# Kernel tuning notes

Measured on AMD Instinct MI355X. Metric: run time of the kernel, lower is better.

The kernel has to match this reference:

```python
import jax, jax.numpy as jnp
import numpy as np


def setup_inputs() -> dict:
    key = jax.random.key(0)
    ks = jax.random.split(key, 7)
    B, V, D, H = 4, 1024, 3, 128
    vertices = jax.random.normal(ks[0], (B, V, D), dtype=jnp.float32)
    # Linear params (x @ W + b convention, W = torch_weight.T)
    W1 = jax.random.normal(ks[1], (2 * D, H), dtype=jnp.float32) * 0.05
    b1 = jnp.zeros((H,), dtype=jnp.float32)
    W2 = jax.random.normal(ks[2], (H, H // 2), dtype=jnp.float32) * 0.05
    b2 = jnp.zeros((H // 2,), dtype=jnp.float32)
    W3 = jax.random.normal(ks[3], (H // 2, 1), dtype=jnp.float32) * 0.05
    b3 = jnp.zeros((1,), dtype=jnp.float32)
    return {"vertices": vertices, "W1": W1, "b1": b1, "W2": W2, "b2": b2, "W3": W3, "b3": b3}


def reference(vertices, W1, b1, W2, b2, W3, b3):
    B, V, D = vertices.shape
    # All unordered pairs (i, j) with i < j -- same order as the nested loop.
    idx_i, idx_j = jnp.triu_indices(V, k=1)  # each [E], E = V*(V-1)/2
    # Pairwise edge features [B, E, 2D] via gather (no Python loop).
    edge_features = jnp.concatenate(
        [vertices[:, idx_i, :], vertices[:, idx_j, :]], axis=-1
    )
    # 3-layer MLP (dropout is identity in eval mode).
    x = jax.nn.relu(edge_features @ W1 + b1)   # [B, E, H]
    x = jax.nn.relu(x @ W2 + b2)               # [B, E, H//2]
    x = x @ W3 + b3                            # [B, E, 1]
    edge_probs = jax.nn.sigmoid(x[..., 0])     # [B, E]
    edge_indices = jnp.stack([idx_i, idx_j], axis=1)  # [E, 2]
    return edge_probs, edge_indices
```

## Files before the change

kernel.cpp:

```cpp
#include <hip/hip_runtime.h>
#include <hip/hip_bf16.h>
#include <math.h>

#define BB 4
#define VV 1024
#define HH 128
#define H2 64
#define EE 523776
#define BE (BB * EE)
#define TPB (EE / 16)
#define NTILES (BE / 16)
#define NTHR 256
#define NBLK 1024

typedef __attribute__((ext_vector_type(8))) short bf16x8;
typedef __attribute__((ext_vector_type(4))) float f32x4;

__device__ __forceinline__ short f2bf(float f) {
    __hip_bfloat16 h = __float2bfloat16(f);
    return *reinterpret_cast<short*>(&h);
}

__global__ __launch_bounds__(NTHR, 3) void edge_mlp_mfma2(
    const float* __restrict__ vertices,
    const float* __restrict__ W1,
    const float* __restrict__ b1,
    const float* __restrict__ W2,
    const float* __restrict__ b2,
    const float* __restrict__ W3,
    const float* __restrict__ b3,
    float* __restrict__ out)
{
    const int lane = threadIdx.x & 63;
    const int col  = lane & 15;
    const int u    = lane >> 4;
    const int wid  = threadIdx.x >> 6;

    const f32x4 zero4 = {0.f, 0.f, 0.f, 0.f};

    bf16x8 A1[4][2];
#pragma unroll
    for (int p = 0; p < 4; ++p)
#pragma unroll
        for (int q = 0; q < 2; ++q) {
            const int h = 32 * p + 8 * (col >> 2) + 4 * q + (col & 3);
#pragma unroll
            for (int r = 0; r < 8; ++r) {
                const int k = 8 * u + r;
                float w = 0.0f;
                if (k < 6)       w = W1[k * HH + h];
                else if (k == 6) w = b1[h];
                A1[p][q][r] = f2bf(w);
            }
        }

    bf16x8 A2[4][4];
#pragma unroll
    for (int mt = 0; mt < 4; ++mt)
#pragma unroll
        for (int p = 0; p < 4; ++p) {
            const int n2 = 16 * mt + col;
#pragma unroll
            for (int r = 0; r < 8; ++r) {
                const int h = 32 * p + 8 * u + r;
                A2[mt][p][r] = f2bf(W2[h * H2 + n2]);
            }
        }

    f32x4 cinit[4];
    float w3c[16];
#pragma unroll
    for (int mt = 0; mt < 4; ++mt)
#pragma unroll
        for (int q = 0; q < 4; ++q) {
            const int n2 = 16 * mt + 4 * u + q;
            cinit[mt][q]    = b2[n2];
            w3c[mt * 4 + q] = W3[n2];
        }
    const float b3v = b3[0];

    const int gw = blockIdx.x * 4 + wid;

    for (int tt = gw; tt < NTILES; tt += NBLK * 4) {
        const int b  = tt / TPB;
        const int e0 = (tt - b * TPB) * 16;
        const int e  = e0 + col;

        const int rr = EE - 1 - e;
        const float sq = sqrtf((float)(8 * rr + 1));
        int m = (int)(0.5f * (sq - 1.0f));
        if ((m + 1) * (m + 2) / 2 <= rr) ++m;
        if (m * (m + 1) / 2 > rr) --m;
        const int pp = rr - m * (m + 1) / 2;
        const int iv = VV - 2 - m;
        const int jv = VV - 1 - pp;

        bf16x8 bf = {0, 0, 0, 0, 0, 0, 0, 0};
        if (u == 0) {
            const float* pvi = vertices + (b * VV + iv) * 3;
            const float* pvj = vertices + (b * VV + jv) * 3;
            bf[0] = f2bf(pvi[0]); bf[1] = f2bf(pvi[1]); bf[2] = f2bf(pvi[2]);
            bf[3] = f2bf(pvj[0]); bf[4] = f2bf(pvj[1]); bf[5] = f2bf(pvj[2]);
            bf[6] = f2bf(1.0f);
        }

        f32x4 d2_0 = cinit[0], d2_1 = cinit[1], d2_2 = cinit[2], d2_3 = cinit[3];

#pragma unroll
        for (int p = 0; p < 4; ++p) {
            f32x4 dA = __builtin_amdgcn_mfma_f32_16x16x32_bf16(A1[p][0], bf, zero4, 0, 0, 0);
            f32x4 dB = __builtin_amdgcn_mfma_f32_16x16x32_bf16(A1[p][1], bf, zero4, 0, 0, 0);
            bf16x8 Bh;
            Bh[0] = f2bf(fmaxf(dA[0], 0.f)); Bh[1] = f2bf(fmaxf(dA[1], 0.f));
            Bh[2] = f2bf(fmaxf(dA[2], 0.f)); Bh[3] = f2bf(fmaxf(dA[3], 0.f));
            Bh[4] = f2bf(fmaxf(dB[0], 0.f)); Bh[5] = f2bf(fmaxf(dB[1], 0.f));
            Bh[6] = f2bf(fmaxf(dB[2], 0.f)); Bh[7] = f2bf(fmaxf(dB[3], 0.f));
            d2_0 = __builtin_amdgcn_mfma_f32_16x16x32_bf16(A2[0][p], Bh, d2_0, 0, 0, 0);
            d2_1 = __builtin_amdgcn_mfma_f32_16x16x32_bf16(A2[1][p], Bh, d2_1, 0, 0, 0);
            d2_2 = __builtin_amdgcn_mfma_f32_16x16x32_bf16(A2[2][p], Bh, d2_2, 0, 0, 0);
            d2_3 = __builtin_amdgcn_mfma_f32_16x16x32_bf16(A2[3][p], Bh, d2_3, 0, 0, 0);
        }

        float acc = 0.f;
#pragma unroll
        for (int q = 0; q < 4; ++q) acc = fmaf(fmaxf(d2_0[q], 0.f), w3c[q],      acc);
#pragma unroll
        for (int q = 0; q < 4; ++q) acc = fmaf(fmaxf(d2_1[q], 0.f), w3c[4 + q],  acc);
#pragma unroll
        for (int q = 0; q < 4; ++q) acc = fmaf(fmaxf(d2_2[q], 0.f), w3c[8 + q],  acc);
#pragma unroll
        for (int q = 0; q < 4; ++q) acc = fmaf(fmaxf(d2_3[q], 0.f), w3c[12 + q], acc);

        acc += __shfl_xor(acc, 16);
        acc += __shfl_xor(acc, 32);

        if (u == 0) {
            const float x = acc + b3v;
            const float prob = __builtin_amdgcn_rcpf(1.0f + __expf(-x));
            out[tt * 16 + col] = prob;
            if (b == 0) {
                *(float2*)(&out[BE + 2 * e]) = make_float2((float)iv, (float)jv);
            }
        }
    }
}

extern "C" void kernel_launch(void* const* d_in, const int* in_sizes, int n_in,
                              void* d_out, int out_size, void* d_ws, size_t ws_size,
                              hipStream_t stream) {
    const float* vertices = (const float*)d_in[0];
    const float* W1 = (const float*)d_in[1];
    const float* b1 = (const float*)d_in[2];
    const float* W2 = (const float*)d_in[3];
    const float* b2 = (const float*)d_in[4];
    const float* W3 = (const float*)d_in[5];
    const float* b3 = (const float*)d_in[6];
    float* out = (float*)d_out;

    edge_mlp_mfma2<<<NBLK, NTHR, 0, stream>>>(vertices, W1, b1, W2, b2, W3, b3, out);
}
```

Measured before the change: 151.1 us.

## Factor layer-1 into per-vertex P/Q projections and map warps to row i

Splits the first linear layer as W1 applied to vertex i plus W1 applied to vertex j, precomputed per vertex (P, Q) in a separate small kernel, so each edge only adds two vectors before ReLU. The layer-1 MFMAs and the per-edge sqrt-based triangular index inversion go away. Each warp now handles one fixed row i and loops over 16-wide column blocks j, and the final 64-to-1 dot product runs as MFMAs with weights held in shared memory. The cost is a second launch, a workspace round trip for P/Q, and load imbalance because rows near i=0 have many more j blocks than rows near the end.

```diff
diff --git a/kernel.cpp b/kernel.cpp
--- a/kernel.cpp
+++ b/kernel.cpp
@@ -8,138 +8,150 @@
 #define H2 64
 #define EE 523776
 #define BE (BB * EE)
-#define TPB (EE / 16)
-#define NTILES (BE / 16)
 #define NTHR 256
 #define NBLK 1024
+#define PQN (BB * VV * HH)
 
 typedef __attribute__((ext_vector_type(8))) short bf16x8;
 typedef __attribute__((ext_vector_type(4))) float f32x4;
+typedef __attribute__((ext_vector_type(4))) unsigned u32x4;
 
 __device__ __forceinline__ short f2bf(float f) {
     __hip_bfloat16 h = __float2bfloat16(f);
     return *reinterpret_cast<short*>(&h);
 }
 
-__global__ __launch_bounds__(NTHR, 3) void edge_mlp_mfma2(
-    const float* __restrict__ vertices,
-    const float* __restrict__ W1,
-    const float* __restrict__ b1,
+__device__ __forceinline__ unsigned pkbf(float lo, float hi) {
+    return __builtin_amdgcn_perm(__float_as_uint(hi), __float_as_uint(lo),
+                                 0x07060302u);
+}
+
+__global__ __launch_bounds__(NTHR) void pq_kernel(
+    const float* __restrict__ vertices, const float* __restrict__ W1,
+    const float* __restrict__ b1, float* __restrict__ P, float* __restrict__ Q)
+{
+    const int t = blockIdx.x * NTHR + threadIdx.x;
+    const int v = t >> 7;
+    const int h = t & 127;
+    const float x = vertices[v * 3 + 0];
+    const float y = vertices[v * 3 + 1];
+    const float z = vertices[v * 3 + 2];
+    P[t] = x * W1[0 * HH + h] + y * W1[1 * HH + h] + z * W1[2 * HH + h];
+    Q[t] = x * W1[3 * HH + h] + y * W1[4 * HH + h] + z * W1[5 * HH + h] + b1[h];
+}
+
+__global__ __launch_bounds__(NTHR, 4) void edge_pq(
+    const float* __restrict__ P,
+    const float* __restrict__ Q,
     const float* __restrict__ W2,
     const float* __restrict__ b2,
     const float* __restrict__ W3,
     const float* __restrict__ b3,
     float* __restrict__ out)
 {
+    __shared__ __align__(16) f32x4  cini[4 * 64];
+    __shared__ __align__(16) bf16x8 wA3[2 * 64];
+
     const int lane = threadIdx.x & 63;
     const int col  = lane & 15;
     const int u    = lane >> 4;
     const int wid  = threadIdx.x >> 6;
 
+    bf16x8 A2r[16];
+#pragma unroll
+    for (int mt = 0; mt < 4; ++mt) {
+        const int n2 = 32 * (mt >> 1) + 8 * (col >> 2) + 4 * (mt & 1) + (col & 3);
+#pragma unroll
+        for (int p = 0; p < 4; ++p) {
+#pragma unroll
+            for (int r = 0; r < 8; ++r)
+                A2r[mt * 4 + p][r] = f2bf(W2[(32 * p + 8 * u + r) * H2 + n2]);
+        }
+    }
+
+    if (wid == 0) {
+#pragma unroll
+        for (int mt = 0; mt < 4; ++mt) {
+            f32x4 c;
+#pragma unroll
+            for (int q = 0; q < 4; ++q)
+                c[q] = b2[32 * (mt >> 1) + 8 * u + 4 * (mt & 1) + q];
+            cini[mt * 64 + lane] = c;
+        }
+    } else if (wid == 1) {
+#pragma unroll
+        for (int t = 0; t < 2; ++t) {
+            bf16x8 a;
+#pragma unroll
+            for (int r = 0; r < 8; ++r) a[r] = f2bf(W3[32 * t + 8 * u + r]);
+            wA3[t * 64 + lane] = a;
+        }
+    }
+    const float b3v = b3[0];
+    __syncthreads();
+
+    const int w = blockIdx.x * 4 + wid;
+    const int b = w >> 10;
+    const int i = w & 1023;
+
+    const float* Pi = P + ((b << 10) + i) * HH;
+    const int ebase = (i * (2 * VV - 1 - i)) >> 1;
+    float* const probout = out + b * EE + ebase - (i + 1);
+    float* const idxout  = out + BE;
+
     const f32x4 zero4 = {0.f, 0.f, 0.f, 0.f};
+    (void)zero4;
 
-    bf16x8 A1[4][2];
+    for (int jb = (i + 1) >> 4; jb < 64; ++jb) {
+        const int j = (jb << 4) + col;
+        const float* Qj = Q + ((b << 10) + (jb << 4) + col) * HH;
+
+        bf16x8 Bf[4];
 #pragma unroll
-    for (int p = 0; p < 4; ++p)
-#pragma unroll
-        for (int q = 0; q < 2; ++q) {
-            const int h = 32 * p + 8 * (col >> 2) + 4 * q + (col & 3);
-#pragma unroll
-            for (int r = 0; r < 8; ++r) {
-                const int k = 8 * u + r;
-                float w = 0.0f;
-                if (k < 6)       w = W1[k * HH + h];
-                else if (k == 6) w = b1[h];
-                A1[p][q][r] = f2bf(w);
-            }
+        for (int p = 0; p < 4; ++p) {
+            const float4 pa = *(const float4*)(Pi + 32 * p + 8 * u);
+            const float4 pb = *(const float4*)(Pi + 32 * p + 8 * u + 4);
+            const float4 qa = *(const float4*)(Qj + 32 * p + 8 * u);
+            const float4 qb = *(const float4*)(Qj + 32 * p + 8 * u + 4);
+            u32x4 rr;
+            rr[0] = pkbf(fmaxf(pa.x + qa.x, 0.f), fmaxf(pa.y + qa.y, 0.f));
+            rr[1] = pkbf(fmaxf(pa.z + qa.z, 0.f), fmaxf(pa.w + qa.w, 0.f));
+            rr[2] = pkbf(fmaxf(pb.x + qb.x, 0.f), fmaxf(pb.y + qb.y, 0.f));
+            rr[3] = pkbf(fmaxf(pb.z + qb.z, 0.f), fmaxf(pb.w + qb.w, 0.f));
+            Bf[p] = __builtin_bit_cast(bf16x8, rr);
         }
 
-    bf16x8 A2[4][4];
+        f32x4 d2[4];
 #pragma unroll
-    for (int mt = 0; mt < 4; ++mt)
+        for (int mt = 0; mt < 4; ++mt) d2[mt] = cini[mt * 64 + lane];
 #pragma unroll
         for (int p = 0; p < 4; ++p) {
-            const int n2 = 16 * mt + col;
 #pragma unroll
-            for (int r = 0; r < 8; ++r) {
-                const int h = 32 * p + 8 * u + r;
-                A2[mt][p][r] = f2bf(W2[h * H2 + n2]);
-            }
+            for (int mt = 0; mt < 4; ++mt)
+                d2[mt] = __builtin_amdgcn_mfma_f32_16x16x32_bf16(
+                    A2r[mt * 4 + p], Bf[p], d2[mt], 0, 0, 0);
         }
 
-    f32x4 cinit[4];
-    float w3c[16];
+        bf16x8 Bh3[2];
 #pragma unroll
-    for (int mt = 0; mt < 4; ++mt)
-#pragma unroll
-        for (int q = 0; q < 4; ++q) {
-            const int n2 = 16 * mt + 4 * u + q;
-            cinit[mt][q]    = b2[n2];
-            w3c[mt * 4 + q] = W3[n2];
+        for (int t = 0; t < 2; ++t) {
+            u32x4 rr;
+            rr[0] = pkbf(fmaxf(d2[2 * t][0], 0.f), fmaxf(d2[2 * t][1], 0.f));
+            rr[1] = pkbf(fmaxf(d2[2 * t][2], 0.f), fmaxf(d2[2 * t][3], 0.f));
+            rr[2] = pkbf(fmaxf(d2[2 * t + 1][0], 0.f), fmaxf(d2[2 * t + 1][1], 0.f));
+            rr[3] = pkbf(fmaxf(d2[2 * t + 1][2], 0.f), fmaxf(d2[2 * t + 1][3], 0.f));
+            Bh3[t] = __builtin_bit_cast(bf16x8, rr);
         }
-    const float b3v = b3[0];
+        f32x4 d3 = {b3v, b3v, b3v, b3v};
+        d3 = __builtin_amdgcn_mfma_f32_16x16x32_bf16(wA3[0 * 64 + lane], Bh3[0], d3, 0, 0, 0);
+        d3 = __builtin_amdgcn_mfma_f32_16x16x32_bf16(wA3[1 * 64 + lane], Bh3[1], d3, 0, 0, 0);
 
-    const int gw = blockIdx.x * 4 + wid;
-
-    for (int tt = gw; tt < NTILES; tt += NBLK * 4) {
-        const int b  = tt / TPB;
-        const int e0 = (tt - b * TPB) * 16;
-        const int e  = e0 + col;
-
-        const int rr = EE - 1 - e;
-        const float sq = sqrtf((float)(8 * rr + 1));
-        int m = (int)(0.5f * (sq - 1.0f));
-        if ((m + 1) * (m + 2) / 2 <= rr) ++m;
-        if (m * (m + 1) / 2 > rr) --m;
-        const int pp = rr - m * (m + 1) / 2;
-        const int iv = VV - 2 - m;
-        const int jv = VV - 1 - pp;
-
-        bf16x8 bf = {0, 0, 0, 0, 0, 0, 0, 0};
-        if (u == 0) {
-            const float* pvi = vertices + (b * VV + iv) * 3;
-            const float* pvj = vertices + (b * VV + jv) * 3;
-            bf[0] = f2bf(pvi[0]); bf[1] = f2bf(pvi[1]); bf[2] = f2bf(pvi[2]);
-            bf[3] = f2bf(pvj[0]); bf[4] = f2bf(pvj[1]); bf[5] = f2bf(pvj[2]);
-            bf[6] = f2bf(1.0f);
-        }
-
-        f32x4 d2_0 = cinit[0], d2_1 = cinit[1], d2_2 = cinit[2], d2_3 = cinit[3];
-
-#pragma unroll
-        for (int p = 0; p < 4; ++p) {
-            f32x4 dA = __builtin_amdgcn_mfma_f32_16x16x32_bf16(A1[p][0], bf, zero4, 0, 0, 0);
-            f32x4 dB = __builtin_amdgcn_mfma_f32_16x16x32_bf16(A1[p][1], bf, zero4, 0, 0, 0);
-            bf16x8 Bh;
-            Bh[0] = f2bf(fmaxf(dA[0], 0.f)); Bh[1] = f2bf(fmaxf(dA[1], 0.f));
-            Bh[2] = f2bf(fmaxf(dA[2], 0.f)); Bh[3] = f2bf(fmaxf(dA[3], 0.f));
-            Bh[4] = f2bf(fmaxf(dB[0], 0.f)); Bh[5] = f2bf(fmaxf(dB[1], 0.f));
-            Bh[6] = f2bf(fmaxf(dB[2], 0.f)); Bh[7] = f2bf(fmaxf(dB[3], 0.f));
-            d2_0 = __builtin_amdgcn_mfma_f32_16x16x32_bf16(A2[0][p], Bh, d2_0, 0, 0, 0);
-            d2_1 = __builtin_amdgcn_mfma_f32_16x16x32_bf16(A2[1][p], Bh, d2_1, 0, 0, 0);
-            d2_2 = __builtin_amdgcn_mfma_f32_16x16x32_bf16(A2[2][p], Bh, d2_2, 0, 0, 0);
-            d2_3 = __builtin_amdgcn_mfma_f32_16x16x32_bf16(A2[3][p], Bh, d2_3, 0, 0, 0);
-        }
-
-        float acc = 0.f;
-#pragma unroll
-        for (int q = 0; q < 4; ++q) acc = fmaf(fmaxf(d2_0[q], 0.f), w3c[q],      acc);
-#pragma unroll
-        for (int q = 0; q < 4; ++q) acc = fmaf(fmaxf(d2_1[q], 0.f), w3c[4 + q],  acc);
-#pragma unroll
-        for (int q = 0; q < 4; ++q) acc = fmaf(fmaxf(d2_2[q], 0.f), w3c[8 + q],  acc);
-#pragma unroll
-        for (int q = 0; q < 4; ++q) acc = fmaf(fmaxf(d2_3[q], 0.f), w3c[12 + q], acc);
-
-        acc += __shfl_xor(acc, 16);
-        acc += __shfl_xor(acc, 32);
-
-        if (u == 0) {
-            const float x = acc + b3v;
-            const float prob = __builtin_amdgcn_rcpf(1.0f + __expf(-x));
-            out[tt * 16 + col] = prob;
+        if (u == 0 && j > i) {
+            const float prob = __builtin_amdgcn_rcpf(1.0f + __expf(-d3[0]));
+            probout[j] = prob;
             if (b == 0) {
-                *(float2*)(&out[BE + 2 * e]) = make_float2((float)iv, (float)jv);
+                const int e = ebase + j - i - 1;
+                *(float2*)(&idxout[2 * e]) = make_float2((float)i, (float)j);
             }
         }
     }
@@ -157,5 +169,9 @@
     const float* b3 = (const float*)d_in[6];
     float* out = (float*)d_out;
 
-    edge_mlp_mfma2<<<NBLK, NTHR, 0, stream>>>(vertices, W1, b1, W2, b2, W3, b3, out);
+    float* P = (float*)d_ws;
+    float* Q = P + PQN;
+
+    pq_kernel<<<PQN / NTHR, NTHR, 0, stream>>>(vertices, W1, b1, P, Q);
+    edge_pq<<<NBLK, NTHR, 0, stream>>>(P, Q, W2, b2, W3, b3, out);
 }
```

After: 532.9 us. 253% more time.

## Move layer-3 to MFMA, stage W1/W3/b2 in LDS, pack bf16 via perm

Applied to the files above, without the earlier changes.

The final 64->1 projection now runs as two bf16 MFMAs on the relu'd layer-2 outputs, replacing the per-lane FMA chain and cross-lane shuffles. To make this work, the W2 output columns are permuted so the layer-2 accumulator layout feeds directly as MFMA B operands. W1, W3 and b2 fragments move from registers into shared memory to cut register pressure. bf16 packing switches to a truncating byte-perm, which changes rounding from round-to-nearest to truncation.

```diff
diff --git a/kernel.cpp b/kernel.cpp
--- a/kernel.cpp
+++ b/kernel.cpp
@@ -12,16 +12,32 @@
 #define NTILES (BE / 16)
 #define NTHR 256
 #define NBLK 1024
+#define NWAVE (NBLK * 4)
 
 typedef __attribute__((ext_vector_type(8))) short bf16x8;
 typedef __attribute__((ext_vector_type(4))) float f32x4;
+typedef __attribute__((ext_vector_type(4))) unsigned u32x4;
 
 __device__ __forceinline__ short f2bf(float f) {
     __hip_bfloat16 h = __float2bfloat16(f);
     return *reinterpret_cast<short*>(&h);
 }
 
-__global__ __launch_bounds__(NTHR, 3) void edge_mlp_mfma2(
+__device__ __forceinline__ unsigned pkbf(float lo, float hi) {
+    return __builtin_amdgcn_perm(__float_as_uint(hi), __float_as_uint(lo),
+                                 0x07060302u);
+}
+
+__device__ __forceinline__ bf16x8 relu_pack(f32x4 a, f32x4 b) {
+    u32x4 r;
+    r[0] = pkbf(fmaxf(a[0], 0.f), fmaxf(a[1], 0.f));
+    r[1] = pkbf(fmaxf(a[2], 0.f), fmaxf(a[3], 0.f));
+    r[2] = pkbf(fmaxf(b[0], 0.f), fmaxf(b[1], 0.f));
+    r[3] = pkbf(fmaxf(b[2], 0.f), fmaxf(b[3], 0.f));
+    return __builtin_bit_cast(bf16x8, r);
+}
+
+__global__ __launch_bounds__(NTHR, 3) void edge_mlp_v11(
     const float* __restrict__ vertices,
     const float* __restrict__ W1,
     const float* __restrict__ b1,
@@ -31,6 +47,9 @@
     const float* __restrict__ b3,
     float* __restrict__ out)
 {
+    __shared__ __align__(16) bf16x8 wA[10 * 64];
+    __shared__ __align__(16) f32x4  wC[4 * 64];
+
     const int lane = threadIdx.x & 63;
     const int col  = lane & 15;
     const int u    = lane >> 4;
@@ -38,50 +57,52 @@
 
     const f32x4 zero4 = {0.f, 0.f, 0.f, 0.f};
 
-    bf16x8 A1[4][2];
+    bf16x8 A2r[16];
 #pragma unroll
-    for (int p = 0; p < 4; ++p)
+    for (int mt = 0; mt < 4; ++mt) {
+        const int n2 = 32 * (mt >> 1) + 8 * (col >> 2) + 4 * (mt & 1) + (col & 3);
 #pragma unroll
-        for (int q = 0; q < 2; ++q) {
-            const int h = 32 * p + 8 * (col >> 2) + 4 * q + (col & 3);
+        for (int p = 0; p < 4; ++p)
+#pragma unroll
+            for (int r = 0; r < 8; ++r)
+                A2r[mt * 4 + p][r] = f2bf(W2[(32 * p + 8 * u + r) * H2 + n2]);
+    }
+
+    for (int f = wid; f < 14; f += 4) {
+        if (f < 8) {
+            const int p = f >> 1, q1 = f & 1;
+            const int h = 32 * p + 8 * (col >> 2) + 4 * q1 + (col & 3);
+            bf16x8 a;
 #pragma unroll
             for (int r = 0; r < 8; ++r) {
                 const int k = 8 * u + r;
                 float w = 0.0f;
                 if (k < 6)       w = W1[k * HH + h];
                 else if (k == 6) w = b1[h];
-                A1[p][q][r] = f2bf(w);
+                a[r] = f2bf(w);
             }
+            wA[f * 64 + lane] = a;
+        } else if (f < 10) {
+            const int t = f - 8;
+            bf16x8 a;
+#pragma unroll
+            for (int r = 0; r < 8; ++r) a[r] = f2bf(W3[32 * t + 8 * u + r]);
+            wA[f * 64 + lane] = a;
+        } else {
+            const int mt = f - 10;
+            f32x4 c;
+#pragma unroll
+            for (int q = 0; q < 4; ++q)
+                c[q] = b2[32 * (mt >> 1) + 8 * u + 4 * (mt & 1) + q];
+            wC[mt * 64 + lane] = c;
         }
-
-    bf16x8 A2[4][4];
-#pragma unroll
-    for (int mt = 0; mt < 4; ++mt)
-#pragma unroll
-        for (int p = 0; p < 4; ++p) {
-            const int n2 = 16 * mt + col;
-#pragma unroll
-            for (int r = 0; r < 8; ++r) {
-                const int h = 32 * p + 8 * u + r;
-                A2[mt][p][r] = f2bf(W2[h * H2 + n2]);
-            }
-        }
-
-    f32x4 cinit[4];
-    float w3c[16];
-#pragma unroll
-    for (int mt = 0; mt < 4; ++mt)
-#pragma unroll
-        for (int q = 0; q < 4; ++q) {
-            const int n2 = 16 * mt + 4 * u + q;
-            cinit[mt][q]    = b2[n2];
-            w3c[mt * 4 + q] = W3[n2];
-        }
+    }
     const float b3v = b3[0];
+    __syncthreads();
 
     const int gw = blockIdx.x * 4 + wid;
 
-    for (int tt = gw; tt < NTILES; tt += NBLK * 4) {
+    for (int tt = gw; tt < NTILES; tt += NWAVE) {
         const int b  = tt / TPB;
         const int e0 = (tt - b * TPB) * 16;
         const int e  = e0 + col;
@@ -95,52 +116,46 @@
         const int iv = VV - 2 - m;
         const int jv = VV - 1 - pp;
 
-        bf16x8 bf = {0, 0, 0, 0, 0, 0, 0, 0};
-        if (u == 0) {
-            const float* pvi = vertices + (b * VV + iv) * 3;
-            const float* pvj = vertices + (b * VV + jv) * 3;
-            bf[0] = f2bf(pvi[0]); bf[1] = f2bf(pvi[1]); bf[2] = f2bf(pvi[2]);
-            bf[3] = f2bf(pvj[0]); bf[4] = f2bf(pvj[1]); bf[5] = f2bf(pvj[2]);
-            bf[6] = f2bf(1.0f);
-        }
+        const float* pvi = vertices + (b * VV + iv) * 3;
+        const float* pvj = vertices + (b * VV + jv) * 3;
+        u32x4 fb;
+        fb[0] = pkbf(pvi[0], pvi[1]);
+        fb[1] = pkbf(pvi[2], pvj[0]);
+        fb[2] = pkbf(pvj[1], pvj[2]);
+        fb[3] = 0x00003F80u;
+        const bf16x8 bfv = __builtin_bit_cast(bf16x8, fb);
 
-        f32x4 d2_0 = cinit[0], d2_1 = cinit[1], d2_2 = cinit[2], d2_3 = cinit[3];
+        f32x4 d2_0 = wC[0 * 64 + lane];
+        f32x4 d2_1 = wC[1 * 64 + lane];
+        f32x4 d2_2 = wC[2 * 64 + lane];
+        f32x4 d2_3 = wC[3 * 64 + lane];
 
 #pragma unroll
         for (int p = 0; p < 4; ++p) {
-            f32x4 dA = __builtin_amdgcn_mfma_f32_16x16x32_bf16(A1[p][0], bf, zero4, 0, 0, 0);
-            f32x4 dB = __builtin_amdgcn_mfma_f32_16x16x32_bf16(A1[p][1], bf, zero4, 0, 0, 0);
-            bf16x8 Bh;
-            Bh[0] = f2bf(fmaxf(dA[0], 0.f)); Bh[1] = f2bf(fmaxf(dA[1], 0.f));
-            Bh[2] = f2bf(fmaxf(dA[2], 0.f)); Bh[3] = f2bf(fmaxf(dA[3], 0.f));
-            Bh[4] = f2bf(fmaxf(dB[0], 0.f)); Bh[5] = f2bf(fmaxf(dB[1], 0.f));
-            Bh[6] = f2bf(fmaxf(dB[2], 0.f)); Bh[7] = f2bf(fmaxf(dB[3], 0.f));
-            d2_0 = __builtin_amdgcn_mfma_f32_16x16x32_bf16(A2[0][p], Bh, d2_0, 0, 0, 0);
-            d2_1 = __builtin_amdgcn_mfma_f32_16x16x32_bf16(A2[1][p], Bh, d2_1, 0, 0, 0);
-            d2_2 = __builtin_amdgcn_mfma_f32_16x16x32_bf16(A2[2][p], Bh, d2_2, 0, 0, 0);
-            d2_3 = __builtin_amdgcn_mfma_f32_16x16x32_bf16(A2[3][p], Bh, d2_3, 0, 0, 0);
+            const bf16x8 a1a = wA[(2 * p + 0) * 64 + lane];
+            const bf16x8 a1b = wA[(2 * p + 1) * 64 + lane];
+            const f32x4 dA = __builtin_amdgcn_mfma_f32_16x16x32_bf16(a1a, bfv, zero4, 0, 0, 0);
+            const f32x4 dB = __builtin_amdgcn_mfma_f32_16x16x32_bf16(a1b, bfv, zero4, 0, 0, 0);
+            const bf16x8 Bh = relu_pack(dA, dB);
+            d2_0 = __builtin_amdgcn_mfma_f32_16x16x32_bf16(A2r[0 * 4 + p], Bh, d2_0, 0, 0, 0);
+            d2_1 = __builtin_amdgcn_mfma_f32_16x16x32_bf16(A2r[1 * 4 + p], Bh, d2_1, 0, 0, 0);
+            d2_2 = __builtin_amdgcn_mfma_f32_16x16x32_bf16(A2r[2 * 4 + p], Bh, d2_2, 0, 0, 0);
+            d2_3 = __builtin_amdgcn_mfma_f32_16x16x32_bf16(A2r[3 * 4 + p], Bh, d2_3, 0, 0, 0);
         }
 
-        float acc = 0.f;
-#pragma unroll
-        for (int q = 0; q < 4; ++q) acc = fmaf(fmaxf(d2_0[q], 0.f), w3c[q],      acc);
-#pragma unroll
-        for (int q = 0; q < 4; ++q) acc = fmaf(fmaxf(d2_1[q], 0.f), w3c[4 + q],  acc);
-#pragma unroll
-        for (int q = 0; q < 4; ++q) acc = fmaf(fmaxf(d2_2[q], 0.f), w3c[8 + q],  acc);
-#pragma unroll
-        for (int q = 0; q < 4; ++q) acc = fmaf(fmaxf(d2_3[q], 0.f), w3c[12 + q], acc);
-
-        acc += __shfl_xor(acc, 16);
-        acc += __shfl_xor(acc, 32);
+        const bf16x8 Bh3_0 = relu_pack(d2_0, d2_1);
+        const bf16x8 Bh3_1 = relu_pack(d2_2, d2_3);
+        const bf16x8 a30 = wA[8 * 64 + lane];
+        const bf16x8 a31 = wA[9 * 64 + lane];
+        f32x4 d3 = {b3v, b3v, b3v, b3v};
+        d3 = __builtin_amdgcn_mfma_f32_16x16x32_bf16(a30, Bh3_0, d3, 0, 0, 0);
+        d3 = __builtin_amdgcn_mfma_f32_16x16x32_bf16(a31, Bh3_1, d3, 0, 0, 0);
 
         if (u == 0) {
-            const float x = acc + b3v;
-            const float prob = __builtin_amdgcn_rcpf(1.0f + __expf(-x));
+            const float prob = __builtin_amdgcn_rcpf(1.0f + __expf(-d3[0]));
             out[tt * 16 + col] = prob;
-            if (b == 0) {
+            if (b == 0)
                 *(float2*)(&out[BE + 2 * e]) = make_float2((float)iv, (float)jv);
-            }
         }
     }
 }
@@ -157,5 +172,5 @@
     const float* b3 = (const float*)d_in[6];
     float* out = (float*)d_out;
 
-    edge_mlp_mfma2<<<NBLK, NTHR, 0, stream>>>(vertices, W1, b1, W2, b2, W3, b3, out);
+    edge_mlp_v11<<<NBLK, NTHR, 0, stream>>>(vertices, W1, b1, W2, b2, W3, b3, out);
 }
```

Measured after the change: 136.5 us. -9.6%, faster.
